# Optimization experiments

Measured on AMD Instinct MI355X. Metric: run time of the kernel, lower is better.

The kernel has to match this reference:

```python
import jax, jax.numpy as jnp
import numpy as np

B, DIM, HID = 16384, 1024, 2048
HALF = DIM // 2
# alternating checkerboard mask: even indices are 'masked' (conditioning) dims
_MASK = np.arange(DIM) % 2 == 0
MASK_IDX = np.nonzero(_MASK)[0]      # dims fed to the MLP (static)
NEG_IDX = np.nonzero(~_MASK)[0]      # dims transformed by the affine coupling (static)


def setup_inputs() -> dict:
    key = jax.random.key(0)
    ks = jax.random.split(key, 8)
    s = 0.02  # small init so exp(s) stays well-behaved
    return {
        "z": jax.random.normal(ks[0], (B, DIM), jnp.float32),
        "log_det": jnp.zeros((B,), jnp.float32),
        "W1": jax.random.normal(ks[1], (HID, HALF), jnp.float32) * s,
        "b1": jax.random.normal(ks[2], (HID,), jnp.float32) * s,
        "W2": jax.random.normal(ks[3], (HID, HID), jnp.float32) * s,
        "b2": jax.random.normal(ks[4], (HID,), jnp.float32) * s,
        "W3": jax.random.normal(ks[5], (DIM, HID), jnp.float32) * s,
        "b3": jax.random.normal(ks[6], (DIM,), jnp.float32) * s,
    }


def reference(z, log_det, W1, b1, W2, b2, W3, b3):
    # gather conditioning dims (static column indices -> jit-friendly)
    zm = z[:, MASK_IDX]                                    # [B, HALF]
    # 3-layer MLP with exact (erf) GELU, matching torch nn.GELU default
    h = jax.nn.gelu(zm @ W1.T + b1, approximate=False)     # [B, HID]
    h = jax.nn.gelu(h @ W2.T + b2, approximate=False)      # [B, HID]
    s_t = h @ W3.T + b3                                    # [B, DIM]
    s, t = s_t[:, :HALF], s_t[:, HALF:]                    # each [B, HALF]
    # affine coupling on the complementary dims, scatter back (forward, inverse=False)
    z_out = z.at[:, NEG_IDX].set(z[:, NEG_IDX] * jnp.exp(s) + t)
    log_det_out = log_det + jnp.sum(s, axis=1)
    return z_out, log_det_out
```

## Files before the change

### kernel.cpp

```cpp
#include <hip/hip_runtime.h>
#include <hip/hip_bf16.h>
#include <cstdint>

typedef __bf16 bf16x8 __attribute__((ext_vector_type(8)));
typedef float  f32x4  __attribute__((ext_vector_type(4)));

struct alignas(4) us2 { unsigned short x, y; };
struct alignas(8) us4 { unsigned short x, y, z, w; };

__device__ __forceinline__ unsigned short f2bf(float f) {
    union { float f; unsigned u; } a; a.f = f;
    unsigned r = a.u + 0x7fffu + ((a.u >> 16) & 1u);
    return (unsigned short)(r >> 16);
}

__device__ __forceinline__ void gl_lds16(const void* g, void* s) {
    __builtin_amdgcn_global_load_lds(
        (const __attribute__((address_space(1))) void*)g,
        (__attribute__((address_space(3))) void*)s, 16, 0, 0);
}

#define SCHEDB()  __builtin_amdgcn_sched_barrier(0)
#define SBAR()    do { SCHEDB(); __builtin_amdgcn_s_barrier(); SCHEDB(); } while (0)
#define WAITLG(N) do { asm volatile("s_waitcnt lgkmcnt(" #N ")" ::: "memory"); SCHEDB(); } while (0)
#define WAITVM(N) do { asm volatile("s_waitcnt vmcnt(" #N ")" ::: "memory"); SCHEDB(); } while (0)

template<int EPI, int K, int N>
__global__ __launch_bounds__(512, 2)
void gemm256(const unsigned short* __restrict__ A,
             const unsigned short* __restrict__ W,
             const float* __restrict__ bias,
             unsigned short* __restrict__ outb,
             float* __restrict__ outf,
             const float* __restrict__ zin,
             float* __restrict__ ldout)
{
    extern __shared__ char smem[];
    constexpr int NH = K / 32;
    constexpr int GX = N / 256;

    const int tid  = threadIdx.x;
    const int lane = tid & 63;
    const int wv   = tid >> 6;
    const int wr   = wv >> 2, wc = wv & 3;

    const int bid = blockIdx.y * GX + blockIdx.x;
    const int nwg = GX * (int)gridDim.y;
    const int swz = (bid & 7) * (nwg >> 3) + (bid >> 3);
    const size_t row0 = (size_t)(swz / GX) * 256;
    const size_t col0 = (size_t)(swz % GX) * 256;

    const int cse = (((tid & 3) ^ ((tid >> 3) & 3)) << 3);
    const unsigned short* ag = A + (row0 + (tid >> 2)) * (size_t)K + cse;
    const unsigned short* bg = W + (col0 + (tid >> 2)) * (size_t)K + cse;

    auto stage = [&](int hh) {
        char* dA = smem + (hh & 3) * 16384 + tid * 16;
        char* dB = dA + 65536;
        const unsigned short* a = ag + (size_t)hh * 32;
        const unsigned short* b = bg + (size_t)hh * 32;
        gl_lds16(a,                     dA);
        gl_lds16(a + (size_t)128 * K,   dA + 8192);
        gl_lds16(b,                     dB);
        gl_lds16(b + (size_t)128 * K,   dB + 8192);
    };

    const int ln15 = lane & 15;
    const int xo   = (((lane >> 4) ^ ((ln15 >> 1) & 3)) << 4);
    const int arow = wr * 128 + ln15;
    const int brow = wc * 64 + ln15;

#define LD(base, row) (*(const bf16x8*)((base) + (size_t)(row) * 64 + xo))

    f32x4 acc[8][4] = {};

    stage(0); stage(1); stage(2);

    for (int h = 0; h < NH; ++h) {
        const char* cA = smem + (h & 3) * 16384;
        const char* cB = cA + 65536;

        if (h < NH - 2)       WAITVM(8);
        else if (h == NH - 2) WAITVM(4);
        else                  WAITVM(0);
        SBAR();

        bf16x8 aF[8], bF[4];
#pragma unroll
        for (int mf = 0; mf < 4; ++mf) aF[mf] = LD(cA, arow + mf * 16);
#pragma unroll
        for (int nf = 0; nf < 4; ++nf) bF[nf] = LD(cB, brow + nf * 16);
        if (h + 3 < NH) stage(h + 3);
        SBAR();
        WAITLG(0);
        __builtin_amdgcn_s_setprio(1);
#pragma unroll
        for (int mf = 0; mf < 4; ++mf)
#pragma unroll
            for (int nf = 0; nf < 4; ++nf)
                acc[mf][nf] = __builtin_amdgcn_mfma_f32_16x16x32_bf16(
                    aF[mf], bF[nf], acc[mf][nf], 0, 0, 0);
        __builtin_amdgcn_s_setprio(0);
        SBAR();

#pragma unroll
        for (int mf = 4; mf < 8; ++mf) aF[mf] = LD(cA, arow + mf * 16);
        SBAR();
        WAITLG(0);
        __builtin_amdgcn_s_setprio(1);
#pragma unroll
        for (int mf = 4; mf < 8; ++mf)
#pragma unroll
            for (int nf = 0; nf < 4; ++nf)
                acc[mf][nf] = __builtin_amdgcn_mfma_f32_16x16x32_bf16(
                    aF[mf], bF[nf], acc[mf][nf], 0, 0, 0);
        __builtin_amdgcn_s_setprio(0);
    }
#undef LD

    const int lq = lane >> 4;
    float bv[4];
#pragma unroll
    for (int nf = 0; nf < 4; ++nf) bv[nf] = bias[col0 + wc * 64 + nf * 16 + ln15];

    if (EPI == 2) {
        const bool odd = (ln15 & 1);
#pragma unroll
        for (int mi = 0; mi < 8; ++mi) {
#pragma unroll
            for (int r = 0; r < 4; ++r) {
                const size_t row = row0 + wr * 128 + mi * 16 + lq * 4 + r;
#pragma unroll
                for (int nf = 0; nf < 4; ++nf) {
                    const size_t col = col0 + wc * 64 + nf * 16 + ln15;
                    float v = acc[mi][nf][r] + bv[nf];
                    float partner = __shfl_xor(v, 1, 64);
                    float zv = zin[row * N + col];
                    float res = odd ? (zv * __expf(partner) + v) : zv;
                    outf[row * N + col] = res;
                }
            }
        }
#pragma unroll
        for (int mi = 0; mi < 8; ++mi) {
#pragma unroll
            for (int r = 0; r < 4; ++r) {
                float sv = 0.f;
#pragma unroll
                for (int nf = 0; nf < 4; ++nf) sv += acc[mi][nf][r] + bv[nf];
                sv = odd ? 0.f : sv;
#pragma unroll
                for (int off = 1; off < 16; off <<= 1) sv += __shfl_xor(sv, off, 64);
                if (ln15 == 0) {
                    const size_t row = row0 + wr * 128 + mi * 16 + lq * 4 + r;
                    atomicAdd(&ldout[row], sv);
                }
            }
        }
    } else {
#pragma unroll
        for (int mi = 0; mi < 8; ++mi) {
#pragma unroll
            for (int r = 0; r < 4; ++r) {
                const size_t row = row0 + wr * 128 + mi * 16 + lq * 4 + r;
#pragma unroll
                for (int nf = 0; nf < 4; ++nf) {
                    const size_t col = col0 + wc * 64 + nf * 16 + ln15;
                    float v = acc[mi][nf][r] + bv[nf];
                    if (EPI == 0) {
                        float g = 0.5f * v * (1.0f + erff(v * 0.70710678118654752f));
                        outb[row * N + col] = f2bf(g);
                    } else {
                        outf[row * N + col] = v;
                    }
                }
            }
        }
    }
}

__global__ void cvt_bf16(const float* __restrict__ in, unsigned short* __restrict__ out, int n4) {
    const int stride = gridDim.x * blockDim.x;
    for (int i = blockIdx.x * blockDim.x + threadIdx.x; i < n4; i += stride) {
        float4 v = ((const float4*)in)[i];
        us4 o{ f2bf(v.x), f2bf(v.y), f2bf(v.z), f2bf(v.w) };
        ((us4*)out)[i] = o;
    }
}

__global__ void cvt_w3i(const float* __restrict__ in, unsigned short* __restrict__ out, int n4) {
    const int stride = gridDim.x * blockDim.x;
    for (int i = blockIdx.x * blockDim.x + threadIdx.x; i < n4; i += stride) {
        int row = i >> 9;
        int c4  = i & 511;
        int srcrow = (row & 1) ? 512 + (row >> 1) : (row >> 1);
        float4 v = ((const float4*)in)[srcrow * 512 + c4];
        us4 o{ f2bf(v.x), f2bf(v.y), f2bf(v.z), f2bf(v.w) };
        ((us4*)out)[i] = o;
    }
}

__global__ void pack_even(const float* __restrict__ z, unsigned short* __restrict__ zm, int n4) {
    const int stride = gridDim.x * blockDim.x;
    for (int i = blockIdx.x * blockDim.x + threadIdx.x; i < n4; i += stride) {
        float4 v = ((const float4*)z)[i];
        us2 o{ f2bf(v.x), f2bf(v.z) };
        ((us2*)zm)[i] = o;
    }
}

__global__ void prep3(const float* __restrict__ b3, float* __restrict__ b3i,
                      const float* __restrict__ ld, float* __restrict__ ldout, int nrow) {
    const int stride = gridDim.x * blockDim.x;
    int i = blockIdx.x * blockDim.x + threadIdx.x;
    if (i < 1024) b3i[i] = b3[(i & 1) ? 512 + (i >> 1) : (i >> 1)];
    for (int r = i; r < nrow; r += stride) ldout[r] = ld[r];
}

extern "C" void kernel_launch(void* const* d_in, const int* in_sizes, int n_in,
                              void* d_out, int out_size, void* d_ws, size_t ws_size,
                              hipStream_t stream)
{
    const float* z  = (const float*)d_in[0];
    const float* ld = (const float*)d_in[1];
    const float* W1 = (const float*)d_in[2];
    const float* b1 = (const float*)d_in[3];
    const float* W2 = (const float*)d_in[4];
    const float* b2 = (const float*)d_in[5];
    const float* W3 = (const float*)d_in[6];
    const float* b3 = (const float*)d_in[7];

    float* out   = (float*)d_out;
    float* zout  = out;
    float* ldout = out + (size_t)16384 * 1024;

    char* w = (char*)d_ws;
    unsigned short* zm  = (unsigned short*)w; w += (size_t)16384 * 512 * 2;
    unsigned short* w1b = (unsigned short*)w; w += (size_t)2048 * 512 * 2;
    unsigned short* w2b = (unsigned short*)w; w += (size_t)2048 * 2048 * 2;
    unsigned short* w3i = (unsigned short*)w; w += (size_t)1024 * 2048 * 2;
    unsigned short* h1  = (unsigned short*)w; w += (size_t)16384 * 2048 * 2;
    unsigned short* h2  = (unsigned short*)w; w += (size_t)16384 * 2048 * 2;
    float*          b3i = (float*)w;          w += 1024 * 4;

    (void)hipFuncSetAttribute((const void*)&gemm256<0, 512,  2048>,
                              hipFuncAttributeMaxDynamicSharedMemorySize, 131072);
    (void)hipFuncSetAttribute((const void*)&gemm256<0, 2048, 2048>,
                              hipFuncAttributeMaxDynamicSharedMemorySize, 131072);
    (void)hipFuncSetAttribute((const void*)&gemm256<2, 2048, 1024>,
                              hipFuncAttributeMaxDynamicSharedMemorySize, 131072);

    cvt_bf16 <<<512,  256, 0, stream>>>(W1, w1b, 2048 * 512 / 4);
    cvt_bf16 <<<2048, 256, 0, stream>>>(W2, w2b, 2048 * 2048 / 4);
    cvt_w3i  <<<1024, 256, 0, stream>>>(W3, w3i, 1024 * 2048 / 4);
    pack_even<<<2048, 256, 0, stream>>>(z, zm, 16384 * 1024 / 4);
    prep3    <<<64,   256, 0, stream>>>(b3, b3i, ld, ldout, 16384);

    gemm256<0, 512,  2048><<<dim3(8, 64), 512, 131072, stream>>>(zm, w1b, b1, h1, nullptr, nullptr, nullptr);
    gemm256<0, 2048, 2048><<<dim3(8, 64), 512, 131072, stream>>>(h1, w2b, b2, h2, nullptr, nullptr, nullptr);
    gemm256<2, 2048, 1024><<<dim3(4, 64), 512, 131072, stream>>>(h2, w3i, b3i, nullptr, zout, z, ldout);
}
```

Measured before the change: 338.4 us.

## Interleave W3 rows in 16-blocks and issue all LDS fragment loads before MFMAs

W3 and b3 rows are now interleaved in blocks of 16 rows instead of alternating single rows. Each lane then holds matching s and t values in adjacent MFMA fragments, so the coupling epilogue no longer needs a cross-lane shuffle for the partner value. It also does float2 loads and stores of the z pairs and folds the log-det reduction into the same loop. In the main loop, the second half of the A fragments is now read before the next stage is issued, with a partial lgkmcnt wait, and two barriers are removed so LDS latency overlaps the first MFMA batch. The cost is more live registers and reliance on the careful wait counts being correct.

```diff
diff --git a/kernel.cpp b/kernel.cpp
--- a/kernel.cpp
+++ b/kernel.cpp
@@ -90,9 +90,13 @@
         for (int mf = 0; mf < 4; ++mf) aF[mf] = LD(cA, arow + mf * 16);
 #pragma unroll
         for (int nf = 0; nf < 4; ++nf) bF[nf] = LD(cB, brow + nf * 16);
+        SCHEDB();
+#pragma unroll
+        for (int mf = 4; mf < 8; ++mf) aF[mf] = LD(cA, arow + mf * 16);
+        SCHEDB();
         if (h + 3 < NH) stage(h + 3);
-        SBAR();
-        WAITLG(0);
+
+        WAITLG(4);
         __builtin_amdgcn_s_setprio(1);
 #pragma unroll
         for (int mf = 0; mf < 4; ++mf)
@@ -101,11 +105,7 @@
                 acc[mf][nf] = __builtin_amdgcn_mfma_f32_16x16x32_bf16(
                     aF[mf], bF[nf], acc[mf][nf], 0, 0, 0);
         __builtin_amdgcn_s_setprio(0);
-        SBAR();
-
-#pragma unroll
-        for (int mf = 4; mf < 8; ++mf) aF[mf] = LD(cA, arow + mf * 16);
-        SBAR();
+
         WAITLG(0);
         __builtin_amdgcn_s_setprio(1);
 #pragma unroll
@@ -124,37 +124,29 @@
     for (int nf = 0; nf < 4; ++nf) bv[nf] = bias[col0 + wc * 64 + nf * 16 + ln15];
 
     if (EPI == 2) {
-        const bool odd = (ln15 & 1);
+        const float2* zin2 = (const float2*)zin;
+        float2*       out2 = (float2*)outf;
 #pragma unroll
         for (int mi = 0; mi < 8; ++mi) {
 #pragma unroll
             for (int r = 0; r < 4; ++r) {
                 const size_t row = row0 + wr * 128 + mi * 16 + lq * 4 + r;
-#pragma unroll
-                for (int nf = 0; nf < 4; ++nf) {
-                    const size_t col = col0 + wc * 64 + nf * 16 + ln15;
-                    float v = acc[mi][nf][r] + bv[nf];
-                    float partner = __shfl_xor(v, 1, 64);
-                    float zv = zin[row * N + col];
-                    float res = odd ? (zv * __expf(partner) + v) : zv;
-                    outf[row * N + col] = res;
+                float sv = 0.f;
+#pragma unroll
+                for (int p = 0; p < 2; ++p) {
+                    float s = acc[mi][2 * p][r] + bv[2 * p];
+                    float t = acc[mi][2 * p + 1][r] + bv[2 * p + 1];
+                    const size_t j = (col0 >> 1) + wc * 32 + p * 16 + ln15;
+                    float2 zv = zin2[row * 512 + j];
+                    float2 o; o.x = zv.x; o.y = zv.y * __expf(s) + t;
+                    out2[row * 512 + j] = o;
+                    sv += s;
                 }
-            }
-        }
-#pragma unroll
-        for (int mi = 0; mi < 8; ++mi) {
-#pragma unroll
-            for (int r = 0; r < 4; ++r) {
-                float sv = 0.f;
-#pragma unroll
-                for (int nf = 0; nf < 4; ++nf) sv += acc[mi][nf][r] + bv[nf];
-                sv = odd ? 0.f : sv;
-#pragma unroll
-                for (int off = 1; off < 16; off <<= 1) sv += __shfl_xor(sv, off, 64);
-                if (ln15 == 0) {
-                    const size_t row = row0 + wr * 128 + mi * 16 + lq * 4 + r;
-                    atomicAdd(&ldout[row], sv);
-                }
+                sv += __shfl_xor(sv, 1, 64);
+                sv += __shfl_xor(sv, 2, 64);
+                sv += __shfl_xor(sv, 4, 64);
+                sv += __shfl_xor(sv, 8, 64);
+                if (ln15 == 0) atomicAdd(&ldout[row], sv);
             }
         }
     } else {
@@ -193,8 +185,9 @@
     for (int i = blockIdx.x * blockDim.x + threadIdx.x; i < n4; i += stride) {
         int row = i >> 9;
         int c4  = i & 511;
-        int srcrow = (row & 1) ? 512 + (row >> 1) : (row >> 1);
-        float4 v = ((const float4*)in)[srcrow * 512 + c4];
+        int q = row >> 5, u = row & 31;
+        int srcrow = (u < 16) ? (q * 16 + u) : (512 + q * 16 + u - 16);
+        float4 v = ((const float4*)in)[(size_t)srcrow * 512 + c4];
         us4 o{ f2bf(v.x), f2bf(v.y), f2bf(v.z), f2bf(v.w) };
         ((us4*)out)[i] = o;
     }
@@ -213,7 +206,10 @@
                       const float* __restrict__ ld, float* __restrict__ ldout, int nrow) {
     const int stride = gridDim.x * blockDim.x;
     int i = blockIdx.x * blockDim.x + threadIdx.x;
-    if (i < 1024) b3i[i] = b3[(i & 1) ? 512 + (i >> 1) : (i >> 1)];
+    if (i < 1024) {
+        int q = i >> 5, u = i & 31;
+        b3i[i] = b3[(u < 16) ? (q * 16 + u) : (512 + q * 16 + u - 16)];
+    }
     for (int r = i; r < nrow; r += stride) ldout[r] = ld[r];
 }
 
```

After: 332.2 us. About the same (-1.8%).
